# Kernel optimization log

Hardware: AMD Instinct MI355X
Metric: run time of the kernel (lower is better)

The kernel has to match this reference:

```python
import jax, jax.numpy as jnp
import numpy as np

SOS_TOKEN = 1
B, H, V, T = 64, 1024, 32000, 40
INPUT_SIZE = 4096


def setup_inputs() -> dict:
    key = jax.random.key(0)
    ks = jax.random.split(key, 12)
    s = 1.0 / np.sqrt(H)
    return {
        "output": jax.random.normal(ks[0], (B, INPUT_SIZE), jnp.float32),
        "h0": jax.random.normal(ks[1], (1, B, H), jnp.float32),
        "c0": jax.random.normal(ks[2], (1, B, H), jnp.float32),
        "target_outputs": jax.random.randint(ks[3], (B, T), 0, V, jnp.int64),
        "target_lengths": jnp.full((B,), T, jnp.int64),
        "embed": jax.random.normal(ks[4], (V, H), jnp.float32),
        "w_ih": jax.random.uniform(ks[5], (4 * H, H), jnp.float32, -s, s),
        "w_hh": jax.random.uniform(ks[6], (4 * H, H), jnp.float32, -s, s),
        "b_ih": jax.random.uniform(ks[7], (4 * H,), jnp.float32, -s, s),
        "b_hh": jax.random.uniform(ks[8], (4 * H,), jnp.float32, -s, s),
        "w_out": jax.random.uniform(ks[9], (V, H), jnp.float32, -s, s),
        "b_out": jax.random.uniform(ks[10], (V,), jnp.float32, -s, s),
    }


def _lstm_cell(x, h, c, w_ih, w_hh, b_ih, b_hh):
    # PyTorch LSTMCell math; gate order i, f, g, o
    gates = x @ w_ih.T + b_ih + h @ w_hh.T + b_hh  # [B, 4H]
    i, f, g, o = jnp.split(gates, 4, axis=-1)
    c2 = jax.nn.sigmoid(f) * c + jax.nn.sigmoid(i) * jnp.tanh(g)
    h2 = jax.nn.sigmoid(o) * jnp.tanh(c2)
    return h2, c2


def reference(output, h0, c0, target_outputs, target_lengths,
              embed, w_ih, w_hh, b_ih, b_hh, w_out, b_out):
    batch = output.shape[0]
    max_lens = int(jnp.max(target_lengths))
    h, c = h0[0], c0[0]  # num_layers=1 -> [B, H]

    # Initial symbol = SOS; initial dec_o = W(embed(SOS)) (no LSTM), as in torch code
    symbol0 = jnp.full((batch,), SOS_TOKEN, dtype=target_outputs.dtype)
    dec_o0 = embed[symbol0] @ w_out.T + b_out  # [B, V]

    def step(carry, _):
        symbol, dec_o, h, c = carry
        # emit current (symbol, dec_o), then decode next
        x = embed[symbol]  # [B, H]
        h2, c2 = _lstm_cell(x, h, c, w_ih, w_hh, b_ih, b_hh)
        dec2 = h2 @ w_out.T + b_out  # [B, V]
        sym2 = jnp.argmax(dec2, axis=-1).astype(symbol.dtype)  # greedy topk(1)
        return (sym2, dec2, h2, c2), (symbol, dec_o)
    (_, _, _, _), (symbols, decs) = jax.lax.scan(
        step, (symbol0, dec_o0, h, c), None, length=max_lens)

    decoder_outs = jnp.transpose(decs, (1, 0, 2))  # [B, T, V]
    symbol_outs = jnp.transpose(symbols, (1, 0))   # [B, T]
    return decoder_outs, symbol_outs
```

## Files before the change

kernel.cpp:

```cpp
#include <hip/hip_runtime.h>

#define Bdim 64
#define Hdim 1024
#define Vdim 32000
#define Tdim 40

typedef __bf16 bf16x8 __attribute__((ext_vector_type(8)));
typedef float  f32x4  __attribute__((ext_vector_type(4)));
typedef unsigned short u16x8 __attribute__((ext_vector_type(8)));
static_assert(sizeof(bf16x8) == 16, "bf16x8 must be 16B");

__device__ __forceinline__ unsigned long long pack_key(float f, int v) {
    unsigned u = __float_as_uint(f);
    u = (u & 0x80000000u) ? ~u : (u | 0x80000000u);
    return ((unsigned long long)u << 32) | (unsigned long long)(0xFFFFFFFFu - (unsigned)v);
}

__device__ __forceinline__ int decode_key(unsigned long long key) {
    return (int)(0xFFFFFFFFu - (unsigned)(key & 0xFFFFFFFFull));
}

__device__ __forceinline__ void gll16(const void* g, void* l) {
    __builtin_amdgcn_global_load_lds(
        (const __attribute__((address_space(1))) void*)g,
        (__attribute__((address_space(3))) void*)l, 16, 0, 0);
}

struct BSplit { unsigned short h, m, l; };

__device__ __forceinline__ BSplit bsplit3v(float x) {
    __bf16 h = (__bf16)x;  float r  = x - (float)h;
    __bf16 m = (__bf16)r;  float r2 = r - (float)m;
    __bf16 l = (__bf16)r2;
    BSplit s;
    s.h = __builtin_bit_cast(unsigned short, h);
    s.m = __builtin_bit_cast(unsigned short, m);
    s.l = __builtin_bit_cast(unsigned short, l);
    return s;
}

__device__ __forceinline__ void bsplit3(float x, unsigned short& a, unsigned short& b,
                                        unsigned short& c) {
    BSplit s = bsplit3v(x);
    a = s.h; b = s.m; c = s.l;
}

template<int NW, int NCH, bool ARGMAX, bool BIAS, bool GATHER>
__device__ __forceinline__ void mm_core(
    unsigned char* sm,
    unsigned long long (*red)[4][16],
    const float* __restrict__ W,
    const unsigned short* __restrict__ Ah,
    const unsigned short* __restrict__ Am,
    const unsigned short* __restrict__ Al,
    const float* __restrict__ Gsrc,
    const unsigned long long* __restrict__ slots_in, int tstep,
    float* __restrict__ sym_dst,
    int n0, const float* __restrict__ bias,
    float* __restrict__ out, size_t out_bstride,
    unsigned long long* __restrict__ slots_out)
{
    constexpr int NT     = NW * 64;
    constexpr int WBYTES = NW * 2048;
    constexpr int BUFSZ  = WBYTES + 12288;

    const int tid  = threadIdx.x;
    const int lane = tid & 63;
    const int wid  = tid >> 6;

    f32x4 acc[4] = {};

    const unsigned char* Wb = (const unsigned char*)W;
    const unsigned char* Apb[3] = {(const unsigned char*)Ah, (const unsigned char*)Am,
                                   (const unsigned char*)Al};

    const int ar = tid >> 2, as = tid & 3;
    const int aswz = as ^ ((ar >> 1) & 3);
    const size_t asrc_off = (size_t)ar * 2048 + (size_t)aswz * 16;
    const size_t aldst    = (size_t)ar * 64 + (size_t)aswz * 16;

    const float* grow = nullptr;
    if constexpr (GATHER) {
        if (tid < 256) {
            int symv = 1;
            if (tstep > 0) {
                unsigned long long key = slots_in[ar];
                symv = decode_key(key);
                if (sym_dst != nullptr && as == 0)
                    sym_dst[ar * Tdim + tstep] = (float)symv;
            }
            grow = Gsrc + (size_t)symv * 1024 + as * 8;
        }
    }

    auto stage = [&](int bufidx, int ch) {
        unsigned char* bb = sm + bufidx * BUFSZ;
        const size_t kb4 = (size_t)ch * 128;
#pragma unroll
        for (int s = 0; s < 2; s++) {
            int gg = tid + NT * s;
            int rw = gg >> 3, cc = gg & 7;
            int sg = cc ^ (rw & 7);
            gll16(Wb + (size_t)rw * 4096 + kb4 + (size_t)sg * 16,
                  bb + ((wid * 64 + NT * s) << 4));
        }
        if constexpr (GATHER) {
            if (tid < 256) {
                const float* p = grow + ch * 32;
                float4 f0 = *(const float4*)(p);
                float4 f1 = *(const float4*)(p + 4);
                u16x8 vh, vm, vl;
                BSplit s0 = bsplit3v(f0.x); vh[0] = s0.h; vm[0] = s0.m; vl[0] = s0.l;
                BSplit s1 = bsplit3v(f0.y); vh[1] = s1.h; vm[1] = s1.m; vl[1] = s1.l;
                BSplit s2 = bsplit3v(f0.z); vh[2] = s2.h; vm[2] = s2.m; vl[2] = s2.l;
                BSplit s3 = bsplit3v(f0.w); vh[3] = s3.h; vm[3] = s3.m; vl[3] = s3.l;
                BSplit s4 = bsplit3v(f1.x); vh[4] = s4.h; vm[4] = s4.m; vl[4] = s4.l;
                BSplit s5 = bsplit3v(f1.y); vh[5] = s5.h; vm[5] = s5.m; vl[5] = s5.l;
                BSplit s6 = bsplit3v(f1.z); vh[6] = s6.h; vm[6] = s6.m; vl[6] = s6.l;
                BSplit s7 = bsplit3v(f1.w); vh[7] = s7.h; vm[7] = s7.m; vl[7] = s7.l;
                *(u16x8*)(bb + WBYTES + aldst)        = vh;
                *(u16x8*)(bb + WBYTES + 4096 + aldst) = vm;
                *(u16x8*)(bb + WBYTES + 8192 + aldst) = vl;
            }
        } else {
            if (tid < 256) {
                const size_t kb2 = (size_t)ch * 64;
#pragma unroll
                for (int pl = 0; pl < 3; pl++)
                    gll16(Apb[pl] + asrc_off + kb2,
                          bb + WBYTES + pl * 4096 + (wid << 10));
            }
        }
    };

    stage(0, 0);
    __syncthreads();

    const int col  = lane & 15;
    const int kg   = lane >> 4;
    const int wrow = wid * 16 + col;
    const int wg0  = (2 * kg) ^ (wrow & 7);
    const int wg1  = (2 * kg + 1) ^ (wrow & 7);

#pragma unroll 2
    for (int ch = 0; ch < NCH; ch++) {
        if (ch + 1 < NCH) stage((ch + 1) & 1, ch + 1);
        unsigned char* base = sm + (ch & 1) * BUFSZ;

        const unsigned char* Wr = base + wrow * 128;
        f32x4 w0 = *(const f32x4*)(Wr + (wg0 << 4));
        f32x4 w1 = *(const f32x4*)(Wr + (wg1 << 4));
        bf16x8 whi, wmid, wlo;
#pragma unroll
        for (int j = 0; j < 4; j++) {
            float x0 = w0[j], x1 = w1[j];
            __bf16 a0 = (__bf16)x0; float r0 = x0 - (float)a0;
            __bf16 b0 = (__bf16)r0; float q0 = r0 - (float)b0;
            whi[j] = a0; wmid[j] = b0; wlo[j] = (__bf16)q0;
            __bf16 a1 = (__bf16)x1; float r1 = x1 - (float)a1;
            __bf16 b1 = (__bf16)r1; float q1 = r1 - (float)b1;
            whi[4 + j] = a1; wmid[4 + j] = b1; wlo[4 + j] = (__bf16)q1;
        }
#pragma unroll
        for (int bt = 0; bt < 4; bt++) {
            const int arow = bt * 16 + col;
            const unsigned char* Ar = base + WBYTES + arow * 64
                                    + ((kg ^ ((arow >> 1) & 3)) << 4);
            bf16x8 ahi = *(const bf16x8*)Ar;
            bf16x8 ami = *(const bf16x8*)(Ar + 4096);
            bf16x8 alo = *(const bf16x8*)(Ar + 8192);
            acc[bt] = __builtin_amdgcn_mfma_f32_16x16x32_bf16(whi,  ahi, acc[bt], 0, 0, 0);
            acc[bt] = __builtin_amdgcn_mfma_f32_16x16x32_bf16(whi,  ami, acc[bt], 0, 0, 0);
            acc[bt] = __builtin_amdgcn_mfma_f32_16x16x32_bf16(wmid, ahi, acc[bt], 0, 0, 0);
            acc[bt] = __builtin_amdgcn_mfma_f32_16x16x32_bf16(whi,  alo, acc[bt], 0, 0, 0);
            acc[bt] = __builtin_amdgcn_mfma_f32_16x16x32_bf16(wlo,  ahi, acc[bt], 0, 0, 0);
            acc[bt] = __builtin_amdgcn_mfma_f32_16x16x32_bf16(wmid, ami, acc[bt], 0, 0, 0);
        }
        __syncthreads();
    }

    const int ncol = n0 + wid * 16 + kg * 4;
    f32x4 bv = {};
    if (BIAS) bv = *(const f32x4*)(bias + ncol);

    unsigned long long bk[4];
#pragma unroll
    for (int bt = 0; bt < 4; bt++) {
        const int b = bt * 16 + col;
        float* op = out + (size_t)b * out_bstride + ncol;
        f32x4 vv;
        unsigned long long best = 0ull;
#pragma unroll
        for (int r = 0; r < 4; r++) {
            float val = acc[bt][r];
            if (BIAS) val += bv[r];
            vv[r] = val;
            if (ARGMAX) {
                unsigned long long key = pack_key(val, ncol + r);
                if (key > best) best = key;
            }
        }
        *(f32x4*)op = vv;
        bk[bt] = best;
    }

    if constexpr (ARGMAX) {
#pragma unroll
        for (int bt = 0; bt < 4; bt++) {
            unsigned long long k = bk[bt];
            unsigned long long o = __shfl_xor(k, 16, 64); if (o > k) k = o;
            o = __shfl_xor(k, 32, 64);                    if (o > k) k = o;
            if (lane < 16) red[wid][bt][lane] = k;
        }
        __syncthreads();
        if (tid < 64) {
            const int bt = tid >> 4, c = tid & 15;
            unsigned long long k = red[0][bt][c];
#pragma unroll
            for (int w = 1; w < NW; w++)
                if (red[w][bt][c] > k) k = red[w][bt][c];
            atomicMax(&slots_out[bt * 16 + c], k);
        }
    }
}

template<bool AM>
__global__ __launch_bounds__(512, 1) void k_logits(
    const float* __restrict__ w_out,
    const unsigned short* __restrict__ ah, const unsigned short* __restrict__ am,
    const unsigned short* __restrict__ al,
    const float* __restrict__ b_out, float* __restrict__ out,
    unsigned long long* __restrict__ slots)
{
    __shared__ __align__(16) unsigned char smem[2][28672];
    __shared__ unsigned long long red[8][4][16];
    const int vb = blockIdx.x * 128;
    mm_core<8, 32, AM, true, false>(&smem[0][0], red,
        w_out + (size_t)vb * Hdim, ah, am, al, nullptr, nullptr, 0, nullptr,
        vb, b_out, out, (size_t)Tdim * Vdim, slots);
}

__global__ __launch_bounds__(256, 2) void k_gates(
    const float* __restrict__ w_ih, const float* __restrict__ w_hh,
    const unsigned short* __restrict__ hh, const unsigned short* __restrict__ hm,
    const unsigned short* __restrict__ hl,
    const float* __restrict__ embed, unsigned long long* __restrict__ slots,
    int t, float* __restrict__ sym_out, float* __restrict__ gp)
{
    __shared__ __align__(16) unsigned char smem[2][20480];
    const int nbi = blockIdx.x, y = blockIdx.y, z = blockIdx.z;
    const float* W = (y ? w_hh : w_ih) + (size_t)nbi * 65536 + z * 256;
    float* gout = gp + (size_t)(y * 4 + z) * (Bdim * 4096);
    if (y)
        mm_core<4, 8, false, false, false>(&smem[0][0], nullptr, W,
            hh + z * 256, hm + z * 256, hl + z * 256, nullptr, nullptr, t, nullptr,
            nbi * 64, nullptr, gout, 4096, nullptr);
    else
        mm_core<4, 8, false, false, true>(&smem[0][0], nullptr, W,
            nullptr, nullptr, nullptr, embed + z * 256, slots, t,
            ((nbi == 0 && z == 0) ? sym_out : nullptr),
            nbi * 64, nullptr, gout, 4096, nullptr);
}

__global__ void k_cell(const float* __restrict__ gp, const float* __restrict__ b_ih,
                       const float* __restrict__ b_hh, float* __restrict__ cbuf,
                       unsigned short* __restrict__ hh, unsigned short* __restrict__ hm,
                       unsigned short* __restrict__ hl,
                       unsigned long long* __restrict__ slots)
{
    const int idx = blockIdx.x * 256 + threadIdx.x;
    const int b = idx >> 10, k = idx & 1023;
    const size_t S = (size_t)Bdim * 4096;
    const size_t base = (size_t)b * 4096;
    float g[4];
#pragma unroll
    for (int q = 0; q < 4; q++) {
        size_t o = base + q * 1024 + k;
        float s = gp[o];
#pragma unroll
        for (int i = 1; i < 8; i++) s += gp[i * S + o];
        g[q] = s + b_ih[q * 1024 + k] + b_hh[q * 1024 + k];
    }
    float si = 1.f / (1.f + expf(-g[0]));
    float sf = 1.f / (1.f + expf(-g[1]));
    float so = 1.f / (1.f + expf(-g[3]));
    float c  = cbuf[idx];
    float c2 = sf * c + si * tanhf(g[2]);
    float h2 = so * tanhf(c2);
    cbuf[idx] = c2;
    unsigned short hs, ms, ls;
    bsplit3(h2, hs, ms, ls);
    const size_t o = (size_t)b * 1024 + k;
    hh[o] = hs; hm[o] = ms; hl[o] = ls;
    if (idx < 64) slots[idx] = 0ull;
}

__global__ void k_init(const float* __restrict__ embed, const float* __restrict__ h0,
                       const float* __restrict__ c0,
                       unsigned short* __restrict__ xsh, unsigned short* __restrict__ xsm,
                       unsigned short* __restrict__ xsl,
                       unsigned short* __restrict__ hh, unsigned short* __restrict__ hm,
                       unsigned short* __restrict__ hl,
                       float* __restrict__ cbuf, float* __restrict__ sym_out,
                       unsigned long long* __restrict__ slots)
{
    const int b = blockIdx.x, t4 = threadIdx.x * 4;
    if (threadIdx.x == 0) { sym_out[b * Tdim] = 1.0f; slots[b] = 0ull; }
    const size_t o = (size_t)b * 1024 + t4;
    ushort4 hi4, mi4, lo4;

    float4 e = *(const float4*)(embed + 1024 + t4);
    bsplit3(e.x, hi4.x, mi4.x, lo4.x);
    bsplit3(e.y, hi4.y, mi4.y, lo4.y);
    bsplit3(e.z, hi4.z, mi4.z, lo4.z);
    bsplit3(e.w, hi4.w, mi4.w, lo4.w);
    *(ushort4*)(xsh + o) = hi4; *(ushort4*)(xsm + o) = mi4; *(ushort4*)(xsl + o) = lo4;

    float4 hv = *(const float4*)(h0 + (size_t)b * 1024 + t4);
    bsplit3(hv.x, hi4.x, mi4.x, lo4.x);
    bsplit3(hv.y, hi4.y, mi4.y, lo4.y);
    bsplit3(hv.z, hi4.z, mi4.z, lo4.z);
    bsplit3(hv.w, hi4.w, mi4.w, lo4.w);
    *(ushort4*)(hh + o) = hi4; *(ushort4*)(hm + o) = mi4; *(ushort4*)(hl + o) = lo4;

    float4 cv = *(const float4*)(c0 + (size_t)b * 1024 + t4);
    *(float4*)(cbuf + (size_t)b * 1024 + t4) = cv;
}

__global__ void k_symfinal(const unsigned long long* __restrict__ slots,
                           float* __restrict__ sym_out)
{
    const int b = threadIdx.x;
    sym_out[b * Tdim + (Tdim - 1)] = (float)decode_key(slots[b]);
}

extern "C" void kernel_launch(void* const* d_in, const int* in_sizes, int n_in,
                              void* d_out, int out_size, void* d_ws, size_t ws_size,
                              hipStream_t stream)
{
    const float* h0    = (const float*)d_in[1];
    const float* c0    = (const float*)d_in[2];
    const float* embed = (const float*)d_in[5];
    const float* w_ih  = (const float*)d_in[6];
    const float* w_hh  = (const float*)d_in[7];
    const float* b_ih  = (const float*)d_in[8];
    const float* b_hh  = (const float*)d_in[9];
    const float* w_out = (const float*)d_in[10];
    const float* b_out = (const float*)d_in[11];

    float* out = (float*)d_out;
    float* sym_out = out + (size_t)Bdim * Tdim * Vdim;

    unsigned short* hh  = (unsigned short*)d_ws;
    unsigned short* hm  = hh + (size_t)Bdim * 1024;
    unsigned short* hl  = hm + (size_t)Bdim * 1024;
    unsigned short* xsh = hl + (size_t)Bdim * 1024;
    unsigned short* xsm = xsh + (size_t)Bdim * 1024;
    unsigned short* xsl = xsm + (size_t)Bdim * 1024;
    float* cbuf = (float*)(xsl + (size_t)Bdim * 1024);
    float* gp   = cbuf + (size_t)Bdim * Hdim;
    unsigned long long* slots = (unsigned long long*)(gp + 8ull * Bdim * 4096);

    k_init<<<Bdim, 256, 0, stream>>>(embed, h0, c0, xsh, xsm, xsl,
                                     hh, hm, hl, cbuf, sym_out, slots);

    k_logits<false><<<Vdim / 128, 512, 0, stream>>>(w_out, xsh, xsm, xsl,
                                                    b_out, out, slots);

    for (int t = 0; t < Tdim - 1; t++) {
        k_gates<<<dim3(64, 2, 4), 256, 0, stream>>>(w_ih, w_hh, hh, hm, hl,
                                                    embed, slots, t, sym_out, gp);
        k_cell<<<Bdim * Hdim / 256, 256, 0, stream>>>(gp, b_ih, b_hh, cbuf,
                                                      hh, hm, hl, slots);
        k_logits<true><<<Vdim / 128, 512, 0, stream>>>(w_out, hh, hm, hl,
                                                       b_out, out + (size_t)(t + 1) * Vdim,
                                                       slots);
    }
    k_symfinal<<<1, 64, 0, stream>>>(slots, sym_out);
}
```

Baseline: 2.606 ms.

## Deepen logits GEMM pipeline to four LDS stages with explicit vmcnt waits

Pulls the logits GEMM out of the shared mm_core into its own kernel. It uses a 4-buffer dynamic-LDS ring, prefetching three chunks ahead, in place of the previous double buffer. Per-wave s_waitcnt vmcnt counts and raw s_barrier with sched_barrier fences let global-to-LDS loads stay in flight across iterations, hiding more memory latency on the w_out stream. In exchange the kernel uses more LDS (about 112KB), and the hand-tuned vmcnt counts are fragile if the number of loads issued per wave changes.

```diff
diff --git a/kernel.cpp b/kernel.cpp
--- a/kernel.cpp
+++ b/kernel.cpp
@@ -25,6 +25,8 @@
         (const __attribute__((address_space(1))) void*)g,
         (__attribute__((address_space(3))) void*)l, 16, 0, 0);
 }
+
+#define VMW(n) asm volatile("s_waitcnt vmcnt(" #n ")" ::: "memory")
 
 struct BSplit { unsigned short h, m, l; };
 
@@ -45,10 +47,159 @@
     a = s.h; b = s.m; c = s.l;
 }
 
-template<int NW, int NCH, bool ARGMAX, bool BIAS, bool GATHER>
+template<bool AM>
+__global__ __launch_bounds__(512, 1) void k_logits(
+    const float* __restrict__ w_out,
+    const unsigned short* __restrict__ ah, const unsigned short* __restrict__ am,
+    const unsigned short* __restrict__ al,
+    const float* __restrict__ b_out, float* __restrict__ out,
+    unsigned long long* __restrict__ slots)
+{
+    constexpr int NW = 8, NCH = 32;
+    constexpr int WBYTES = NW * 2048;
+    constexpr int BUFSZ  = WBYTES + 12288;
+    extern __shared__ __align__(16) unsigned char smem[];
+    __shared__ unsigned long long red[NW][4][16];
+
+    const int tid  = threadIdx.x;
+    const int lane = tid & 63;
+    const int wid  = tid >> 6;
+    const int vb   = blockIdx.x * 128;
+
+    const unsigned char* Wb = (const unsigned char*)(w_out + (size_t)vb * Hdim);
+    const unsigned char* Apb[3] = {(const unsigned char*)ah, (const unsigned char*)am,
+                                   (const unsigned char*)al};
+
+    f32x4 acc[4] = {};
+
+    const int ar = tid >> 2, as = tid & 3;
+    const int aswz = as ^ ((ar >> 1) & 3);
+    const size_t asrc_off = (size_t)ar * 2048 + (size_t)aswz * 16;
+
+    auto stage = [&](int bufidx, int ch) {
+        unsigned char* bb = smem + bufidx * BUFSZ;
+        const size_t kb4 = (size_t)ch * 128;
+#pragma unroll
+        for (int s = 0; s < 2; s++) {
+            int gg = tid + 512 * s;
+            int rw = gg >> 3, cc = gg & 7;
+            int sg = cc ^ (rw & 7);
+            gll16(Wb + (size_t)rw * 4096 + kb4 + (size_t)sg * 16,
+                  bb + ((wid * 64 + 512 * s) << 4));
+        }
+        if (tid < 256) {
+            const size_t kb2 = (size_t)ch * 64;
+#pragma unroll
+            for (int pl = 0; pl < 3; pl++)
+                gll16(Apb[pl] + asrc_off + kb2, bb + WBYTES + pl * 4096 + (wid << 10));
+        }
+    };
+
+    stage(0, 0); stage(1, 1); stage(2, 2);
+
+    const int col  = lane & 15;
+    const int kg   = lane >> 4;
+    const int wrow = wid * 16 + col;
+    const int wg0  = (2 * kg) ^ (wrow & 7);
+    const int wg1  = (2 * kg + 1) ^ (wrow & 7);
+
+#pragma unroll 2
+    for (int ch = 0; ch < NCH; ch++) {
+        if (ch + 3 < NCH) stage((ch + 3) & 3, ch + 3);
+        const int k = (NCH - 1 - ch < 3) ? (NCH - 1 - ch) : 3;
+        if (wid < 4) {
+            if (k == 3) VMW(15); else if (k == 2) VMW(10);
+            else if (k == 1) VMW(5); else VMW(0);
+        } else {
+            if (k == 3) VMW(6); else if (k == 2) VMW(4);
+            else if (k == 1) VMW(2); else VMW(0);
+        }
+        __builtin_amdgcn_sched_barrier(0);
+        __builtin_amdgcn_s_barrier();
+        __builtin_amdgcn_sched_barrier(0);
+
+        const unsigned char* base = smem + (ch & 3) * BUFSZ;
+
+        const unsigned char* Wr = base + wrow * 128;
+        f32x4 w0 = *(const f32x4*)(Wr + (wg0 << 4));
+        f32x4 w1 = *(const f32x4*)(Wr + (wg1 << 4));
+        bf16x8 whi, wmid, wlo;
+#pragma unroll
+        for (int j = 0; j < 4; j++) {
+            float x0 = w0[j], x1 = w1[j];
+            __bf16 a0 = (__bf16)x0; float r0 = x0 - (float)a0;
+            __bf16 b0 = (__bf16)r0; float q0 = r0 - (float)b0;
+            whi[j] = a0; wmid[j] = b0; wlo[j] = (__bf16)q0;
+            __bf16 a1 = (__bf16)x1; float r1 = x1 - (float)a1;
+            __bf16 b1 = (__bf16)r1; float q1 = r1 - (float)b1;
+            whi[4 + j] = a1; wmid[4 + j] = b1; wlo[4 + j] = (__bf16)q1;
+        }
+#pragma unroll
+        for (int bt = 0; bt < 4; bt++) {
+            const int arow = bt * 16 + col;
+            const unsigned char* Ar = base + WBYTES + arow * 64
+                                    + ((kg ^ ((arow >> 1) & 3)) << 4);
+            bf16x8 ahi = *(const bf16x8*)Ar;
+            bf16x8 ami = *(const bf16x8*)(Ar + 4096);
+            bf16x8 alo = *(const bf16x8*)(Ar + 8192);
+            acc[bt] = __builtin_amdgcn_mfma_f32_16x16x32_bf16(whi,  ahi, acc[bt], 0, 0, 0);
+            acc[bt] = __builtin_amdgcn_mfma_f32_16x16x32_bf16(whi,  ami, acc[bt], 0, 0, 0);
+            acc[bt] = __builtin_amdgcn_mfma_f32_16x16x32_bf16(wmid, ahi, acc[bt], 0, 0, 0);
+            acc[bt] = __builtin_amdgcn_mfma_f32_16x16x32_bf16(whi,  alo, acc[bt], 0, 0, 0);
+            acc[bt] = __builtin_amdgcn_mfma_f32_16x16x32_bf16(wlo,  ahi, acc[bt], 0, 0, 0);
+            acc[bt] = __builtin_amdgcn_mfma_f32_16x16x32_bf16(wmid, ami, acc[bt], 0, 0, 0);
+        }
+        __builtin_amdgcn_sched_barrier(0);
+        __builtin_amdgcn_s_barrier();
+        __builtin_amdgcn_sched_barrier(0);
+    }
+
+    const int ncol = vb + wid * 16 + kg * 4;
+    f32x4 bv = *(const f32x4*)(b_out + ncol);
+
+    unsigned long long bk[4];
+#pragma unroll
+    for (int bt = 0; bt < 4; bt++) {
+        const int b = bt * 16 + col;
+        float* op = out + (size_t)b * ((size_t)Tdim * Vdim) + ncol;
+        f32x4 vv;
+        unsigned long long best = 0ull;
+#pragma unroll
+        for (int r = 0; r < 4; r++) {
+            float val = acc[bt][r] + bv[r];
+            vv[r] = val;
+            if (AM) {
+                unsigned long long key = pack_key(val, ncol + r);
+                if (key > best) best = key;
+            }
+        }
+        *(f32x4*)op = vv;
+        bk[bt] = best;
+    }
+
+    if constexpr (AM) {
+#pragma unroll
+        for (int bt = 0; bt < 4; bt++) {
+            unsigned long long k = bk[bt];
+            unsigned long long o = __shfl_xor(k, 16, 64); if (o > k) k = o;
+            o = __shfl_xor(k, 32, 64);                    if (o > k) k = o;
+            if (lane < 16) red[wid][bt][lane] = k;
+        }
+        __syncthreads();
+        if (tid < 64) {
+            const int bt = tid >> 4, c = tid & 15;
+            unsigned long long k = red[0][bt][c];
+#pragma unroll
+            for (int w = 1; w < NW; w++)
+                if (red[w][bt][c] > k) k = red[w][bt][c];
+            atomicMax(&slots[bt * 16 + c], k);
+        }
+    }
+}
+
+template<int NW, int NCH, bool BIAS, bool GATHER>
 __device__ __forceinline__ void mm_core(
     unsigned char* sm,
-    unsigned long long (*red)[4][16],
     const float* __restrict__ W,
     const unsigned short* __restrict__ Ah,
     const unsigned short* __restrict__ Am,
@@ -57,8 +208,7 @@
     const unsigned long long* __restrict__ slots_in, int tstep,
     float* __restrict__ sym_dst,
     int n0, const float* __restrict__ bias,
-    float* __restrict__ out, size_t out_bstride,
-    unsigned long long* __restrict__ slots_out)
+    float* __restrict__ out, size_t out_bstride)
 {
     constexpr int NT     = NW * 64;
     constexpr int WBYTES = NW * 2048;
@@ -183,61 +333,19 @@
     f32x4 bv = {};
     if (BIAS) bv = *(const f32x4*)(bias + ncol);
 
-    unsigned long long bk[4];
 #pragma unroll
     for (int bt = 0; bt < 4; bt++) {
         const int b = bt * 16 + col;
         float* op = out + (size_t)b * out_bstride + ncol;
         f32x4 vv;
-        unsigned long long best = 0ull;
 #pragma unroll
         for (int r = 0; r < 4; r++) {
             float val = acc[bt][r];
             if (BIAS) val += bv[r];
             vv[r] = val;
-            if (ARGMAX) {
-                unsigned long long key = pack_key(val, ncol + r);
-                if (key > best) best = key;
-            }
         }
         *(f32x4*)op = vv;
-        bk[bt] = best;
-    }
-
-    if constexpr (ARGMAX) {
-#pragma unroll
-        for (int bt = 0; bt < 4; bt++) {
-            unsigned long long k = bk[bt];
-            unsigned long long o = __shfl_xor(k, 16, 64); if (o > k) k = o;
-            o = __shfl_xor(k, 32, 64);                    if (o > k) k = o;
-            if (lane < 16) red[wid][bt][lane] = k;
-        }
-        __syncthreads();
-        if (tid < 64) {
-            const int bt = tid >> 4, c = tid & 15;
-            unsigned long long k = red[0][bt][c];
-#pragma unroll
-            for (int w = 1; w < NW; w++)
-                if (red[w][bt][c] > k) k = red[w][bt][c];
-            atomicMax(&slots_out[bt * 16 + c], k);
-        }
-    }
-}
-
-template<bool AM>
-__global__ __launch_bounds__(512, 1) void k_logits(
-    const float* __restrict__ w_out,
-    const unsigned short* __restrict__ ah, const unsigned short* __restrict__ am,
-    const unsigned short* __restrict__ al,
-    const float* __restrict__ b_out, float* __restrict__ out,
-    unsigned long long* __restrict__ slots)
-{
-    __shared__ __align__(16) unsigned char smem[2][28672];
-    __shared__ unsigned long long red[8][4][16];
-    const int vb = blockIdx.x * 128;
-    mm_core<8, 32, AM, true, false>(&smem[0][0], red,
-        w_out + (size_t)vb * Hdim, ah, am, al, nullptr, nullptr, 0, nullptr,
-        vb, b_out, out, (size_t)Tdim * Vdim, slots);
+    }
 }
 
 __global__ __launch_bounds__(256, 2) void k_gates(
@@ -252,14 +360,14 @@
     const float* W = (y ? w_hh : w_ih) + (size_t)nbi * 65536 + z * 256;
     float* gout = gp + (size_t)(y * 4 + z) * (Bdim * 4096);
     if (y)
-        mm_core<4, 8, false, false, false>(&smem[0][0], nullptr, W,
+        mm_core<4, 8, false, false>(&smem[0][0], W,
             hh + z * 256, hm + z * 256, hl + z * 256, nullptr, nullptr, t, nullptr,
-            nbi * 64, nullptr, gout, 4096, nullptr);
+            nbi * 64, nullptr, gout, 4096);
     else
-        mm_core<4, 8, false, false, true>(&smem[0][0], nullptr, W,
+        mm_core<4, 8, false, true>(&smem[0][0], W,
             nullptr, nullptr, nullptr, embed + z * 256, slots, t,
             ((nbi == 0 && z == 0) ? sym_out : nullptr),
-            nbi * 64, nullptr, gout, 4096, nullptr);
+            nbi * 64, nullptr, gout, 4096);
 }
 
 __global__ void k_cell(const float* __restrict__ gp, const float* __restrict__ b_ih,
@@ -361,20 +469,21 @@
     float* gp   = cbuf + (size_t)Bdim * Hdim;
     unsigned long long* slots = (unsigned long long*)(gp + 8ull * Bdim * 4096);
 
+    constexpr size_t LOGITS_LDS = 4 * 28672;
+
     k_init<<<Bdim, 256, 0, stream>>>(embed, h0, c0, xsh, xsm, xsl,
                                      hh, hm, hl, cbuf, sym_out, slots);
 
-    k_logits<false><<<Vdim / 128, 512, 0, stream>>>(w_out, xsh, xsm, xsl,
-                                                    b_out, out, slots);
+    k_logits<false><<<Vdim / 128, 512, LOGITS_LDS, stream>>>(w_out, xsh, xsm, xsl,
+                                                             b_out, out, slots);
 
     for (int t = 0; t < Tdim - 1; t++) {
         k_gates<<<dim3(64, 2, 4), 256, 0, stream>>>(w_ih, w_hh, hh, hm, hl,
                                                     embed, slots, t, sym_out, gp);
         k_cell<<<Bdim * Hdim / 256, 256, 0, stream>>>(gp, b_ih, b_hh, cbuf,
                                                       hh, hm, hl, slots);
-        k_logits<true><<<Vdim / 128, 512, 0, stream>>>(w_out, hh, hm, hl,
-                                                       b_out, out + (size_t)(t + 1) * Vdim,
-                                                       slots);
+        k_logits<true><<<Vdim / 128, 512, LOGITS_LDS, stream>>>(
+            w_out, hh, hm, hl, b_out, out + (size_t)(t + 1) * Vdim, slots);
     }
     k_symfinal<<<1, 64, 0, stream>>>(slots, sym_out);
 }
```

After: 2.650 ms. About the same (+1.7%).
